# Performance work log

Measured on AMD Instinct MI355X. Metric: run time of the kernel, lower is better.

The kernel has to match this reference:

```python
import jax, jax.numpy as jnp
import numpy as np

N_SAMPLES = 32768
WINDOW = 2048
HOP = WINDOW // 2
N_FRAMES = N_SAMPLES // HOP  # 32 resonance frames
BASE_RES = 0.5
RES_SPAN = 1.0 - BASE_RES
RES_FACTOR = 0.9
N_RES = 32
EXPR = 4
CPD = 16
N_COEFFS = WINDOW // 2 + 1  # 1025


def interpolate_last_axis(x, new_size):
    # linear interpolation along last axis (align_corners=False semantics)
    old = x.shape[-1]
    pos = (jnp.arange(new_size, dtype=jnp.float32) + 0.5) * (old / new_size) - 0.5
    pos = jnp.clip(pos, 0.0, old - 1.0)
    lo = jnp.floor(pos).astype(jnp.int32)
    hi = jnp.minimum(lo + 1, old - 1)
    w = pos - lo.astype(jnp.float32)
    return x[..., lo] * (1.0 - w) + x[..., hi] * w


def overlap_add(frames):
    # frames: (..., n_frames, window); hop = window//2; output (..., n_frames*hop)
    *lead, nf, w = frames.shape
    hop = w // 2
    a = frames[..., :hop]
    b = frames[..., hop:]
    b = jnp.concatenate([jnp.zeros_like(b[..., :1, :]), b[..., :-1, :]], axis=-2)
    return (a + b).reshape(*lead, nf * hop)


def freq_domain_transfer_function_to_resonance(window_size, decay_coeffs, n_frames, start_phase, start_mags):
    # decay_coeffs/start_phase/start_mags: (nr, expr, n_coeffs); log-space decay scan
    log_decay = jnp.log(decay_coeffs + 1e-12)[..., None, :]  # (nr, expr, 1, nc)
    shape = log_decay.shape[:-2] + (n_frames, log_decay.shape[-1])
    cum = jnp.cumsum(jnp.broadcast_to(log_decay, shape), axis=-2)  # decay^(f+1)
    mags = jnp.exp(cum) * start_mags[..., None, :]
    spec = mags * jnp.exp(1j * start_phase[..., None, :])
    frames = jnp.fft.irfft(spec, n=window_size, axis=-1)  # (nr, expr, n_frames, window)
    t = jnp.arange(window_size, dtype=jnp.float32)
    hann = 0.5 - 0.5 * jnp.cos(2.0 * jnp.pi * t / window_size)
    return overlap_add(frames * hann)  # (nr, expr, n_frames*hop)


def unit_norm(x):
    return x / (jnp.linalg.norm(x, axis=-1, keepdims=True) + 1e-8)


def fft_convolve(a, b):
    n = a.shape[-1]
    fa = jnp.fft.rfft(a, n=2 * n, axis=-1)
    fb = jnp.fft.rfft(b, n=2 * n, axis=-1)
    return jnp.fft.irfft(fa * fb, n=2 * n, axis=-1)[..., :n]


def setup_inputs() -> dict:
    key = jax.random.key(0)
    ks = jax.random.split(key, 10)
    control_signal = jax.random.normal(ks[0], (2, 4, CPD, 128), dtype=jnp.float32)
    deformations = jax.random.normal(ks[1], (2, 4, EXPR, 128), dtype=jnp.float32) * 0.1
    router = jax.random.uniform(ks[2], (CPD, N_RES), minval=-1.0, maxval=1.0)

    def init_resonance(k):
        k1, k2 = jax.random.split(k)
        res = jax.random.uniform(k1, (N_RES, N_COEFFS, 1), minval=0.01, maxval=1.0)
        deform = jax.random.uniform(k2, (1, N_COEFFS, EXPR), minval=-0.02, maxval=0.02)
        return res + deform

    amp = init_resonance(ks[3])
    phase = init_resonance(ks[4])
    decay = init_resonance(ks[5])
    gains = jax.random.uniform(ks[6], (N_RES, 1), minval=0.01, maxval=1.1)
    return {"control_signal": control_signal, "deformations": deformations,
            "router": router, "amp": amp, "phase": phase, "decay": decay, "gains": gains}


def reference(control_signal, deformations, router, amp, phase, decay, gains):
    b, e, cpd, frames = control_signal.shape
    nr = router.shape[1]
    # route control plane -> resonances: (b,e,nr,frames)
    routed = jnp.einsum('becf,cr->berf', control_signal, router)
    before_upsample = routed
    # (nr, n_coeffs, expr) -> (nr, expr, n_coeffs)
    amp_t = jnp.transpose(amp, (0, 2, 1))
    phase_t = jnp.transpose(phase, (0, 2, 1))
    decay_t = jnp.transpose(decay, (0, 2, 1))
    d_coeffs = BASE_RES + jax.nn.sigmoid(decay_t) * RES_SPAN * RES_FACTOR
    res = freq_domain_transfer_function_to_resonance(
        WINDOW, d_coeffs, N_FRAMES, jnp.tanh(phase_t) * jnp.pi, jnp.abs(amp_t))
    res = unit_norm(res)[None, None]  # (1,1,nr,expr,N)
    routed_up = interpolate_last_axis(routed[:, :, :, None, :], N_SAMPLES)  # (b,e,nr,1,N)
    noise = jax.random.uniform(jax.random.key(123), routed_up.shape, minval=-1.0, maxval=1.0)
    routed_up = routed_up * noise
    conv = fft_convolve(routed_up, res)  # (b,e,nr,expr,N)
    d = deformations.at[:, :, 0, :].add(1.0)  # base deformation favors first expressivity
    d = jax.nn.softmax(d, axis=2)[:, :, None, :, :]  # (b,e,1,expr,def_frames)
    d = interpolate_last_axis(d, N_SAMPLES)
    x = jnp.sum(d * conv, axis=-2)  # mix over expressivity -> (b,e,nr,N)
    summed = jnp.tanh(x * jnp.abs(gains).reshape(1, 1, nr, 1))
    summed = jnp.sum(summed, axis=-2, keepdims=True)  # (b,e,1,N)
    return summed, before_upsample
```

## Files before the change

### kernel.cpp

```cpp
#include <hip/hip_runtime.h>
#include <hip/hip_fp16.h>
#include <stdint.h>


#define PI_F     3.14159265358979323846f
#define TWOPI_F  6.28318530717958647692f
#define UNIT64K  (TWOPI_F/65536.0f)
#define UNIT2K   (TWOPI_F/2048.0f)
#define SCALE64K (1.0f/65536.0f)
#define SK3(i)   ((i) + 3*((i) >> 4))
#define RPH 308
#define SKP(i)   ((i) + 4*((i) >> 4))
#define RPW 328

__device__ __forceinline__ float2 cmul(float2 a, float2 b){
  return make_float2(a.x*b.x - a.y*b.y, a.x*b.y + a.y*b.x);
}

__device__ __forceinline__ float2 twid(uint32_t e, float unit, float sign){
  float ang = (float)e * unit;
  float sn, cn;
  __sincosf(ang, &sn, &cn);
  return make_float2(cn, sign*sn);
}

__device__ __forceinline__ float2 mulnegi(float2 w){ return make_float2(w.y, -w.x); }
__device__ __forceinline__ float2 mulposi(float2 w){ return make_float2(-w.y, w.x); }

__device__ __forceinline__ void bfly_fwd(float2& u, float2& v, float2 w){
  float2 d = make_float2(u.x - v.x, u.y - v.y);
  u = make_float2(u.x + v.x, u.y + v.y);
  v = cmul(d, w);
}

__device__ __forceinline__ uint32_t rotl32(uint32_t v, int r){
  return (v << r) | (v >> (32 - r));
}

__device__ __forceinline__ void threefry2x32(uint32_t c0, uint32_t c1,
                                             uint32_t& o0, uint32_t& o1){
  const uint32_t k0 = 0u, k1 = 123u;
  const uint32_t k2 = 0x1BD11BDAu ^ k0 ^ k1;
  const uint32_t ks[3] = {k0, k1, k2};
  uint32_t x0 = c0 + k0, x1 = c1 + k1;
#pragma unroll
  for (int i = 0; i < 5; i++){
    if ((i & 1) == 0){
      x0 += x1; x1 = rotl32(x1,13); x1 ^= x0;
      x0 += x1; x1 = rotl32(x1,15); x1 ^= x0;
      x0 += x1; x1 = rotl32(x1,26); x1 ^= x0;
      x0 += x1; x1 = rotl32(x1, 6); x1 ^= x0;
    } else {
      x0 += x1; x1 = rotl32(x1,17); x1 ^= x0;
      x0 += x1; x1 = rotl32(x1,29); x1 ^= x0;
      x0 += x1; x1 = rotl32(x1,16); x1 ^= x0;
      x0 += x1; x1 = rotl32(x1,24); x1 ^= x0;
    }
    x0 += ks[(i+1)%3];
    x1 += ks[(i+2)%3] + (uint32_t)(i+1);
  }
  o0 = x0; o1 = x1;
}

__device__ __forceinline__ float jax_noise(uint32_t p){
  uint32_t b0, b1;
  threefry2x32(0u, p, b0, b1);
  uint32_t bits = b0 ^ b1;
  float u = __uint_as_float((bits >> 9) | 0x3f800000u) - 1.0f;
  return fmaxf(-1.0f, u*2.0f - 1.0f);
}

__device__ __forceinline__ void interp128(int t, int& lo, int& hi, float& w){
  float posf = ((float)t + 0.5f) * (1.0f/256.0f) - 0.5f;
  posf = fminf(fmaxf(posf, 0.0f), 127.0f);
  lo = (int)posf;
  hi = lo + 1; if (hi > 127) hi = 127;
  w = posf - (float)lo;
}

__device__ __forceinline__ __half2 u2h(uint32_t u){
  union { uint32_t u; __half2 h; } x; x.u = u; return x.h;
}
__device__ __forceinline__ uint32_t h2u(__half2 h){
  union { uint32_t u; __half2 h; } x; x.h = h; return x.u;
}
__device__ __forceinline__ constexpr int sw4(int k){ return ((k & 3) << 2) | (k >> 2); }
__device__ __forceinline__ constexpr int br4(int x){
  return ((x & 1) << 3) | ((x & 2) << 1) | ((x & 4) >> 1) | ((x & 8) >> 3);
}

__device__ __forceinline__ void cws(float2& u, const float c, const float s){
  const float x = u.x*c - u.y*s;
  u.y = u.x*s + u.y*c;
  u.x = x;
}
__device__ __forceinline__ void cwv(float2& u, const float2 w){
  const float x = u.x*w.x - u.y*w.y;
  u.y = u.x*w.y + u.y*w.x;
  u.x = x;
}

__device__ __forceinline__ void dft4(float2& a, float2& b, float2& c, float2& d,
                                     const float sgn){
  float2 t0 = make_float2(a.x + c.x, a.y + c.y);
  float2 t1 = make_float2(a.x - c.x, a.y - c.y);
  float2 t2 = make_float2(b.x + d.x, b.y + d.y);
  float2 t3 = make_float2(b.x - d.x, b.y - d.y);
  float2 i3 = make_float2(-sgn*t3.y, sgn*t3.x);
  a = make_float2(t0.x + t2.x, t0.y + t2.y);
  c = make_float2(t0.x - t2.x, t0.y - t2.y);
  b = make_float2(t1.x + i3.x, t1.y + i3.y);
  d = make_float2(t1.x - i3.x, t1.y - i3.y);
}

#define DFT16_TW(d, sgn) do { \
  const float C1_ = 0.92387953251128674f, S1_ = 0.38268343236508978f; \
  const float C2_ = 0.70710678118654752f; \
  cws(d[5],  C1_,  (sgn)*S1_); \
  cws(d[6],  C2_,  (sgn)*C2_); \
  cws(d[7],  S1_,  (sgn)*C1_); \
  cws(d[9],  C2_,  (sgn)*C2_); \
  cws(d[10], 0.0f, (sgn)); \
  cws(d[11], -C2_, (sgn)*C2_); \
  cws(d[13], S1_,  (sgn)*C1_); \
  cws(d[14], -C2_, (sgn)*C2_); \
  cws(d[15], -C1_, -(sgn)*S1_); \
} while(0)

__device__ __forceinline__ void dft16(float2* d, const float sgn){
#pragma unroll
  for (int nb = 0; nb < 4; nb++) dft4(d[nb], d[nb+4], d[nb+8], d[nb+12], sgn);
  DFT16_TW(d, sgn);
#pragma unroll
  for (int ka = 0; ka < 4; ka++) dft4(d[4*ka], d[4*ka+1], d[4*ka+2], d[4*ka+3], sgn);
}
__device__ __forceinline__ void dft16b(float2* d, const float sgn){
#pragma unroll
  for (int nb = 0; nb < 4; nb++) dft4(d[4*nb], d[4*nb+1], d[4*nb+2], d[4*nb+3], sgn);
  DFT16_TW(d, sgn);
#pragma unroll
  for (int ka = 0; ka < 4; ka++) dft4(d[ka], d[ka+4], d[ka+8], d[ka+12], sgn);
}

__device__ __forceinline__ void pass1_fwd(__half2* buf, const float2* twl, const int t){
  const int row = t >> 4, L = t & 15;
  __half2* BR = buf + row*RPW;
  float2 d[16];
#pragma unroll
  for (int H = 0; H < 16; H++) d[H] = __half22float2(BR[L + 20*H]);
  dft16(d, -1.0f);
#pragma unroll
  for (int k1 = 0; k1 < 16; k1++){
    float2 y = d[sw4(k1)];
    cwv(y, twl[(L*k1) & 255]);
    BR[L + 20*k1] = __floats2half2_rn(y.x, y.y);
  }
}

__global__ void k_routed(const float* __restrict__ ctrl, const float* __restrict__ defm,
                         const float* __restrict__ router,
                         float* __restrict__ w_routed, float* __restrict__ w_sm,
                         float* __restrict__ out1){
  int idx = blockIdx.x*blockDim.x + threadIdx.x;
  if (idx < 32768){
    int f = idx & 127, r = (idx >> 7) & 31, be = idx >> 12;
    float acc = 0.0f;
#pragma unroll
    for (int c = 0; c < 16; c++)
      acc += ctrl[(be*16 + c)*128 + f] * router[c*32 + r];
    w_routed[idx] = acc;
    out1[idx] = acc;
  } else if (idx < 32768 + 1024){
    int j = idx - 32768;
    int f = j & 127, be = j >> 7;
    float v[4];
#pragma unroll
    for (int x = 0; x < 4; x++)
      v[x] = defm[(be*4 + x)*128 + f] + (x == 0 ? 1.0f : 0.0f);
    float mx = fmaxf(fmaxf(v[0], v[1]), fmaxf(v[2], v[3]));
    float s = 0.0f;
#pragma unroll
    for (int x = 0; x < 4; x++){ v[x] = expf(v[x] - mx); s += v[x]; }
#pragma unroll
    for (int x = 0; x < 4; x++) w_sm[(be*4 + x)*128 + f] = v[x]/s;
  }
}

__global__ void k_frames(const float* __restrict__ amp, const float* __restrict__ phase,
                         const float* __restrict__ decay, float2* __restrict__ w_fr){
  const int wg = blockIdx.x;
  const int f = wg & 31;
  const int rp = wg >> 5;
  const int p = rp & 1;
  const int r = rp >> 1;
  const int t = threadIdx.x;
  __shared__ float2 buf[2048];

  for (int k = t; k <= 1024; k += 256){
    float2 S[2];
#pragma unroll
    for (int d = 0; d < 2; d++){
      const int x = 2*p + d;
      const int base = (r*1025 + k)*4 + x;
      float a  = fabsf(amp[base]);
      float ph = tanhf(phase[base]) * PI_F;
      float sg = 1.0f / (1.0f + expf(-decay[base]));
      float dc = 0.5f + 0.45f * sg;
      float mag = expf(logf(dc + 1e-12f) * (float)(f+1)) * a;
      float snv, csv;
      sincosf(ph, &snv, &csv);
      float re = mag * csv, im = mag * snv;
      if (k == 0 || k == 1024) im = 0.0f;
      S[d] = make_float2(re, im);
    }
    buf[__brev((uint32_t)k) >> 21] =
        make_float2(S[0].x - S[1].y, S[0].y + S[1].x);
    if (k >= 1 && k <= 1023)
      buf[__brev((uint32_t)(2048 - k)) >> 21] =
          make_float2(S[0].x + S[1].y, -S[0].y + S[1].x);
  }
  __syncthreads();
  for (int s = 10; s >= 0; s--){
    const int ls = 10 - s;
    const int hl = 1 << ls;
    for (int bi = t; bi < 1024; bi += 256){
      const int g = bi >> ls, j = bi & (hl - 1);
      const int i0 = g*2*hl + j, i1 = i0 + hl;
      float2 pp = buf[i0], qq = buf[i1];
      float2 w = twid((uint32_t)(j << s), UNIT2K, +1.0f);
      float2 v = cmul(qq, w);
      buf[i0] = make_float2(pp.x+v.x, pp.y+v.y);
      buf[i1] = make_float2(pp.x-v.x, pp.y-v.y);
    }
    __syncthreads();
  }
  float2* O = w_fr + (size_t)wg*2048;
  for (int u = t; u < 2048; u += 256){
    float hann = 0.5f - 0.5f*cosf(TWOPI_F * (float)u / 2048.0f);
    float sc = (1.0f/2048.0f) * hann;
    O[u] = make_float2(buf[u].x*sc, buf[u].y*sc);
  }
}

__global__ void k_ola(const float2* __restrict__ w_fr, float* __restrict__ w_resT,
                      float* __restrict__ w_sumsq){
  const int wg = blockIdx.x;
  const int cq = wg & 7;
  const int rp = wg >> 3;
  const int c0 = cq*32;
  const int r = rp >> 1, p = rp & 1;
  const int ch0 = r*4 + p*2;
  const int t = threadIdx.x;
  __shared__ float tx[32][129], ty[32][129];
  __shared__ float red[2][256];
  const float2* F = w_fr + (size_t)rp*32*2048;
  float acc0 = 0.0f, acc1 = 0.0f;
#pragma unroll
  for (int it = 0; it < 16; it++){
    const int idx = it*256 + t;
    const int cp = idx & 31, m = idx >> 5;
    const int n = c0 + cp + 256*m;
    const int f = n >> 10, u = n & 1023;
    float2 a = F[(size_t)f*2048 + u];
    float vx = a.x, vy = a.y;
    if (f > 0){
      float2 b = F[(size_t)(f-1)*2048 + u + 1024];
      vx += b.x; vy += b.y;
    }
    tx[cp][m] = vx; ty[cp][m] = vy;
    acc0 += vx*vx; acc1 += vy*vy;
  }
  red[0][t] = acc0; red[1][t] = acc1;
  __syncthreads();
#pragma unroll
  for (int it = 0; it < 16; it++){
    const int idx = it*256 + t;
    const int m = idx & 127, cp = idx >> 7;
    w_resT[(size_t)ch0*32768 + (size_t)(c0+cp)*128 + m]     = tx[cp][m];
    w_resT[(size_t)(ch0+1)*32768 + (size_t)(c0+cp)*128 + m] = ty[cp][m];
  }
  for (int off = 128; off > 0; off >>= 1){
    __syncthreads();
    if (t < off){ red[0][t] += red[0][t+off]; red[1][t] += red[1][t+off]; }
  }
  if (t == 0){
    atomicAdd(&w_sumsq[ch0],     red[0][0]);
    atomicAdd(&w_sumsq[ch0 + 1], red[1][0]);
  }
}

__global__ void k_norm(const float* __restrict__ w_sumsq, float* __restrict__ w_invnorm){
  const int s = threadIdx.x;
  if (s < 128) w_invnorm[s] = 1.0f/(sqrtf(w_sumsq[s]) + 1e-8f);
}

__global__ void k_fwdA(const int mode, const float* __restrict__ w_resT,
                       const float* __restrict__ w_invnorm,
                       const float* __restrict__ w_routed,
                       __half2* __restrict__ outh){
  const int wg = blockIdx.x;
  const int cq = wg & 63;
  const int sig = wg >> 6;
  const int c0 = cq*4;
  const int t = threadIdx.x;
  __shared__ __half2 buf[4][RPH];
  if (mode == 0){
    const int rr = sig >> 1, pq = sig & 1;
    const int ch0 = rr*4 + pq*2;
    const float inv0 = w_invnorm[ch0], inv1 = w_invnorm[ch0+1];
#pragma unroll
    for (int i = 0; i < 2; i++){
      const int j = i*256 + t;
      const int cc = j & 3, m = j >> 2;
      const int c = c0 + cc;
      float vx = w_resT[(size_t)ch0*32768 + c*128 + m] * inv0;
      float vy = w_resT[(size_t)(ch0+1)*32768 + c*128 + m] * inv1;
      buf[cc][SK3(m)] = __floats2half2_rn(vx, vy);
      buf[cc][SK3(m + 128)] = __floats2half2_rn(0.0f, 0.0f);
    }
  } else {
    const float* rp = w_routed + sig*128;
#pragma unroll
    for (int i = 0; i < 2; i++){
      const int j = i*256 + t;
      const int cc = j & 3, m = j >> 2;
      const int c = c0 + cc;
      const int n = c + 256*m;
      int lo, hi; float w;
      interp128(n, lo, hi, w);
      float rv = rp[lo]*(1.0f - w) + rp[hi]*w;
      float vx = rv * jax_noise((uint32_t)sig*32768u + (uint32_t)n);
      buf[cc][SK3(m)] = __floats2half2_rn(vx, 0.0f);
      buf[cc][SK3(m + 128)] = __floats2half2_rn(0.0f, 0.0f);
    }
  }
  __syncthreads();
  const int row = t >> 6, q = t & 63;
  for (int sp = 0; sp < 4; sp++){
    const int s  = 2*sp;
    const int hh = 1 << (6 - 2*sp);
    const int hl = hh << 1;
    const int lj = 6 - 2*sp;
    const int j = q & (hh - 1), g = q >> lj;
    const int base = g*2*hl + j;
    const uint32_t e = (uint32_t)(c0 + row) + 256u*(uint32_t)j;
    __half2* B = buf[row];
    const int i0 = SK3(base), i1 = SK3(base+hh), i2 = SK3(base+hl), i3 = SK3(base+hl+hh);
    float2 u0 = __half22float2(B[i0]);
    float2 u1 = __half22float2(B[i1]);
    float2 u2 = __half22float2(B[i2]);
    float2 u3 = __half22float2(B[i3]);
    float2 wA0 = twid((e << s) & 0xFFFFu, UNIT64K, -1.0f);
    float2 wA1 = mulnegi(wA0);
    float2 wB  = cmul(wA0, wA0);
    bfly_fwd(u0, u2, wA0);
    bfly_fwd(u1, u3, wA1);
    bfly_fwd(u0, u1, wB);
    bfly_fwd(u2, u3, wB);
    B[i0] = __floats2half2_rn(u0.x, u0.y);
    B[i1] = __floats2half2_rn(u1.x, u1.y);
    B[i2] = __floats2half2_rn(u2.x, u2.y);
    B[i3] = __floats2half2_rn(u3.x, u3.y);
    __syncthreads();
  }
#pragma unroll
  for (int i = 0; i < 4; i++){
    const int cc = i, m = t;
    outh[(size_t)sig*65536 + (size_t)(c0+cc)*256 + m] = buf[cc][SK3(m)];
  }
}

__global__ __launch_bounds__(256, 4)
void k_fwdB(const __half2* __restrict__ spech, __half2* __restrict__ resp_t){
  const int wg = blockIdx.x;
  const int mq = wg & 15;
  const int sig = wg >> 4;
  const int m16 = mq*16;
  const int t = threadIdx.x;
  __shared__ alignas(16) __half2 buf[16*RPW];
  __shared__ float2 twl[256];
  twl[t] = twid((uint32_t)t << 8, UNIT64K, -1.0f);
  const __half2* base = spech + (size_t)sig*65536;
  {
    const int mm = t & 15, q = t >> 4;
    __half2* BR = buf + mm*RPW;
#pragma unroll
    for (int i = 0; i < 16; i++)
      BR[20*i + q] = base[(size_t)(16*i + q)*256 + m16 + mm];
  }
  __syncthreads();
  pass1_fwd(buf, twl, t);
  __syncthreads();
  {
    const int k1 = t >> 4, row = t & 15;
    __half2* BG = buf + row*RPW + 20*k1;
    float2 v[16];
#pragma unroll
    for (int cc = 0; cc < 4; cc++){
      const uint4 ld = *reinterpret_cast<const uint4*>(BG + 4*cc);
      v[4*cc+0] = __half22float2(u2h(ld.x));
      v[4*cc+1] = __half22float2(u2h(ld.y));
      v[4*cc+2] = __half22float2(u2h(ld.z));
      v[4*cc+3] = __half22float2(u2h(ld.w));
    }
    dft16(v, -1.0f);
    uint4* O4 = reinterpret_cast<uint4*>(resp_t + (((size_t)sig*16 + mq)*256 + t)*16);
#pragma unroll
    for (int cc = 0; cc < 4; cc++){
      uint4 st;
      st.x = h2u(__floats2half2_rn(v[4*cc+0].x, v[4*cc+0].y));
      st.y = h2u(__floats2half2_rn(v[4*cc+1].x, v[4*cc+1].y));
      st.z = h2u(__floats2half2_rn(v[4*cc+2].x, v[4*cc+2].y));
      st.w = h2u(__floats2half2_rn(v[4*cc+3].x, v[4*cc+3].y));
      O4[cc] = st;
    }
  }
}

__global__ __launch_bounds__(256, 4)
void k_conv(const __half2* __restrict__ ruspec,
            const __half2* __restrict__ resp_t,
            __half2* __restrict__ chunkbuf, const int gbase){
  const int wg = blockIdx.x;
  const int mq = wg & 15;
  const int p  = (wg >> 4) & 1;
  const int gl = wg >> 5;
  const int g = gbase + gl;
  const int r = g & 31;
  const int m16 = mq*16;
  const int t = threadIdx.x;
  __shared__ alignas(16) __half2 buf[16*RPW];
  __shared__ float2 twl[256];
  twl[t] = twid((uint32_t)t << 8, UNIT64K, -1.0f);

  {
    const uint4* A4 = reinterpret_cast<const uint4*>(
        ruspec + (size_t)g*65536 + (size_t)t*256 + m16);
    uint4 a0 = A4[0], a1 = A4[1], a2 = A4[2], a3 = A4[3];
    const int cs = SKP(t);
    uint32_t w[16];
    w[0]=a0.x; w[1]=a0.y; w[2]=a0.z; w[3]=a0.w;
    w[4]=a1.x; w[5]=a1.y; w[6]=a1.z; w[7]=a1.w;
    w[8]=a2.x; w[9]=a2.y; w[10]=a2.z; w[11]=a2.w;
    w[12]=a3.x; w[13]=a3.y; w[14]=a3.z; w[15]=a3.w;
#pragma unroll
    for (int mm = 0; mm < 16; mm++)
      buf[mm*RPW + cs] = u2h(w[mm]);
  }
  __syncthreads();
  pass1_fwd(buf, twl, t);
  __syncthreads();
  {
    const int k1 = t >> 4, row = t & 15;
    __half2* BG = buf + row*RPW + 20*k1;
    float2 v[16];
#pragma unroll
    for (int cc = 0; cc < 4; cc++){
      const uint4 ld = *reinterpret_cast<const uint4*>(BG + 4*cc);
      v[4*cc+0] = __half22float2(u2h(ld.x));
      v[4*cc+1] = __half22float2(u2h(ld.y));
      v[4*cc+2] = __half22float2(u2h(ld.z));
      v[4*cc+3] = __half22float2(u2h(ld.w));
    }
    const uint4* Bt = reinterpret_cast<const uint4*>(
        resp_t + (((size_t)(r*2 + p)*16 + mq)*256 + t)*16);
    uint4 b0 = Bt[0], b1 = Bt[1], b2 = Bt[2], b3 = Bt[3];
    dft16(v, -1.0f);
    uint32_t bw[16];
    bw[0]=b0.x; bw[1]=b0.y; bw[2]=b0.z; bw[3]=b0.w;
    bw[4]=b1.x; bw[5]=b1.y; bw[6]=b1.z; bw[7]=b1.w;
    bw[8]=b2.x; bw[9]=b2.y; bw[10]=b2.z; bw[11]=b2.w;
    bw[12]=b3.x; bw[13]=b3.y; bw[14]=b3.z; bw[15]=b3.w;
#pragma unroll
    for (int pp = 0; pp < 16; pp++){
      const float2 b = __half22float2(u2h(bw[pp]));
      const float zx = v[pp].x, zy = v[pp].y;
      v[pp] = make_float2((zx*b.x - zy*b.y)*SCALE64K,
                          (zx*b.y + zy*b.x)*SCALE64K);
    }
    dft16b(v, +1.0f);
    __half2 h[16];
#pragma unroll
    for (int n2 = 0; n2 < 16; n2++){
      float2 m = v[n2];
      const float2 w = twl[(n2*k1) & 255];
      const float x = m.x*w.x + m.y*w.y;
      m.y = -m.x*w.y + m.y*w.x;
      m.x = x;
      h[n2] = __floats2half2_rn(m.x, m.y);
    }
#pragma unroll
    for (int cc = 0; cc < 4; cc++){
      uint4 st;
      st.x = h2u(h[4*cc+0]);
      st.y = h2u(h[4*cc+1]);
      st.z = h2u(h[4*cc+2]);
      st.w = h2u(h[4*cc+3]);
      *reinterpret_cast<uint4*>(BG + 4*cc) = st;
    }
  }
  __syncthreads();
  {
    const int row = t >> 4, L = t & 15;
    __half2* BR = buf + row*RPW;
    float2 d[16];
#pragma unroll
    for (int k1 = 0; k1 < 16; k1++) d[k1] = __half22float2(BR[L + 20*k1]);
    dft16(d, +1.0f);
#pragma unroll
    for (int H = 0; H < 16; H++){
      const float2 x = d[sw4(H)];
      BR[L + 20*H] = __floats2half2_rn(x.x, x.y);
    }
  }
  __syncthreads();
  {
    uint4* O4 = reinterpret_cast<uint4*>(
        chunkbuf + (size_t)(gl*2 + p)*65536 + (size_t)t*256 + m16);
    const int cs = SKP(t);
#pragma unroll
    for (int q4 = 0; q4 < 4; q4++){
      uint4 st;
      st.x = h2u(buf[(4*q4+0)*RPW + cs]);
      st.y = h2u(buf[(4*q4+1)*RPW + cs]);
      st.z = h2u(buf[(4*q4+2)*RPW + cs]);
      st.w = h2u(buf[(4*q4+3)*RPW + cs]);
      O4[q4] = st;
    }
  }
}

__global__ __launch_bounds__(256, 4)
void k_invA_w(const __half2* __restrict__ chunkbuf, const int gbase,
              const float* __restrict__ w_sm, const float* __restrict__ gains,
              float* __restrict__ out0){
  const int wg = blockIdx.x;
  const int c8 = wg & 31;
  const int gl = wg >> 5;
  const int g = gbase + gl;
  const int r = g & 31, be = g >> 5;
  const int c0 = c8*8;
  const int t = threadIdx.x;
  __shared__ alignas(16) __half2 buf[16*RPW];
  __shared__ float sm_lds[512];
  sm_lds[t]       = w_sm[be*512 + t];
  sm_lds[256 + t] = w_sm[be*512 + 256 + t];

  const int row = t >> 4;
  const int p   = row >> 3;
  const int cc  = row & 7;
  const int c   = c0 + cc;
  {
    const int u = t & 15;
    const uint4* C4 = reinterpret_cast<const uint4*>(
        chunkbuf + (size_t)(gl*2 + p)*65536 + (size_t)c*256 + 16*br4(u));
    uint4 z0 = C4[0], z1 = C4[1], z2 = C4[2], z3 = C4[3];
    uint32_t zw[16];
    zw[0]=z0.x; zw[1]=z0.y; zw[2]=z0.z; zw[3]=z0.w;
    zw[4]=z1.x; zw[5]=z1.y; zw[6]=z1.z; zw[7]=z1.w;
    zw[8]=z2.x; zw[9]=z2.y; zw[10]=z2.z; zw[11]=z2.w;
    zw[12]=z3.x; zw[13]=z3.y; zw[14]=z3.z; zw[15]=z3.w;
    const float2 wstep = twid((uint32_t)(16*c) & 0xFFFFu, UNIT64K, +1.0f);
    float2 w = make_float2(1.0f, 0.0f);
    float2 d[16];
#pragma unroll
    for (int rh = 0; rh < 16; rh++){
      d[rh] = cmul(__half22float2(u2h(zw[br4(rh)])), w);
      w = cmul(w, wstep);
    }
    dft16(d, +1.0f);
    __half2* BR = buf + row*RPW;
#pragma unroll
    for (int mL = 0; mL < 16; mL++){
      const float2 s = d[sw4(mL)];
      BR[20*mL + u] = __floats2half2_rn(s.x, s.y);
    }
  }
  __syncthreads();
  const int mL = t & 15;
  float2 v[16];
  {
    const __half2* BG = buf + row*RPW + 20*mL;
#pragma unroll
    for (int q4 = 0; q4 < 4; q4++){
      const uint4 ld = *reinterpret_cast<const uint4*>(BG + 4*q4);
      v[4*q4+0] = __half22float2(u2h(ld.x));
      v[4*q4+1] = __half22float2(u2h(ld.y));
      v[4*q4+2] = __half22float2(u2h(ld.z));
      v[4*q4+3] = __half22float2(u2h(ld.w));
    }
  }
  __syncthreads();
  {
    const float2 wstep = twid((uint32_t)(c + 256*mL) & 0xFFFFu, UNIT64K, +1.0f);
    float2 w = wstep;
#pragma unroll
    for (int kL2 = 1; kL2 < 16; kL2++){
      v[kL2] = cmul(v[kL2], w);
      w = cmul(w, wstep);
    }
    dft16(v, +1.0f);
    __half2* BR = buf + row*RPW;
#pragma unroll
    for (int mH = 0; mH < 8; mH++){
      const float2 x = v[sw4(mH)];
      BR[mL + 20*mH] = __floats2half2_rn(x.x, x.y);
    }
  }
  __syncthreads();
  const float gv = fabsf(gains[r]);
#pragma unroll
  for (int it = 0; it < 4; it++){
    const int li = t + it*256;
    const int cc2 = li & 7, m = li >> 3;
    const int tt = c0 + cc2 + 256*m;
    int lo, hi; float w;
    interp128(tt, lo, hi, w);
    const int cell = (m & 15) + 20*(m >> 4);
    float2 z0 = __half22float2(buf[cc2*RPW + cell]);
    float2 z1 = __half22float2(buf[(8 + cc2)*RPW + cell]);
    float dw0 = sm_lds[0*128 + lo]*(1.0f - w) + sm_lds[0*128 + hi]*w;
    float dw1 = sm_lds[1*128 + lo]*(1.0f - w) + sm_lds[1*128 + hi]*w;
    float dw2 = sm_lds[2*128 + lo]*(1.0f - w) + sm_lds[2*128 + hi]*w;
    float dw3 = sm_lds[3*128 + lo]*(1.0f - w) + sm_lds[3*128 + hi]*w;
    float val = dw0*z0.x + dw1*z0.y + dw2*z1.x + dw3*z1.y;
    atomicAdd(&out0[(size_t)be*32768 + tt], tanhf(val*gv));
  }
}

extern "C" void kernel_launch(void* const* d_in, const int* in_sizes, int n_in,
                              void* d_out, int out_size, void* d_ws, size_t ws_size,
                              hipStream_t stream){
  const float* ctrl   = (const float*)d_in[0];
  const float* defm   = (const float*)d_in[1];
  const float* router = (const float*)d_in[2];
  const float* amp    = (const float*)d_in[3];
  const float* phase  = (const float*)d_in[4];
  const float* decay  = (const float*)d_in[5];
  const float* gains  = (const float*)d_in[6];
  float* out = (float*)d_out;
  float* ws  = (float*)d_ws;

  float*   w_resT    = ws;
  float*   w_routed  = ws + 4194304;
  float*   w_sm      = ws + 4227072;
  float*   w_invnorm = ws + 4231168;
  float*   w_sumsq   = ws + 4231296;
  __half2* ruspec_h  = (__half2*)(ws + 4231424);
  __half2* resp_h    = (__half2*)(ws + 21008640);
  __half2* chunk_h   = (__half2*)(ws + 25202944);
  const size_t base_f = 25202944;
  float2* w_fr       = (float2*)ruspec_h;
  __half2* resp_t    = (__half2*)w_resT;

  int G = 0;
  for (int gg = 128; gg >= 1; gg >>= 1){
    size_t need = (base_f + (size_t)gg*131072) * sizeof(float);
    if (need <= ws_size){ G = gg; break; }
  }

  hipMemsetAsync(d_out, 0, 262144*sizeof(float), stream);
  k_routed<<<132, 256, 0, stream>>>(ctrl, defm, router, w_routed, w_sm, out + 262144);
  if (G == 0) return;

  hipMemsetAsync(w_sumsq, 0, 128*sizeof(float), stream);
  k_frames<<<2048, 256, 0, stream>>>(amp, phase, decay, w_fr);
  k_ola<<<512, 256, 0, stream>>>(w_fr, w_resT, w_sumsq);
  k_norm<<<1, 128, 0, stream>>>(w_sumsq, w_invnorm);
  k_fwdA<<<64*64, 256, 0, stream>>>(0, w_resT, w_invnorm, w_routed, resp_h);
  k_fwdB<<<64*16, 256, 0, stream>>>(resp_h, resp_t);
  k_fwdA<<<256*64, 256, 0, stream>>>(1, w_resT, w_invnorm, w_routed, ruspec_h);
  for (int gb = 0; gb < 256; gb += G){
    k_conv<<<G*32, 256, 0, stream>>>(ruspec_h, resp_t, chunk_h, gb);
    k_invA_w<<<G*32, 256, 0, stream>>>(chunk_h, gb, w_sm, gains, out);
  }
}
```

Measured before the change: 343.8 us.

## Rewrite k_fwdA as register radix-16 two-pass FFT over 16 columns per block

Replaces the shared-memory radix-4 butterfly loop (four passes with a barrier each, one sincos per butterfly) in k_fwdA with a register-resident radix-16 DFT pair. Each thread does a 16-point DFT with incremental twiddles, one shared-memory transpose, a second 16-point DFT, and vectorised uint4 stores. Each block now covers 16 columns instead of 4, so the grid shrinks fourfold. This cuts barriers, LDS traffic and transcendental calls, at the cost of higher register pressure (launch bounds 256,4) and twiddles that accumulate by repeated multiplication, which slightly changes rounding.

```diff
diff --git a/kernel.cpp b/kernel.cpp
--- a/kernel.cpp
+++ b/kernel.cpp
@@ -8,8 +8,6 @@
 #define UNIT64K  (TWOPI_F/65536.0f)
 #define UNIT2K   (TWOPI_F/2048.0f)
 #define SCALE64K (1.0f/65536.0f)
-#define SK3(i)   ((i) + 3*((i) >> 4))
-#define RPH 308
 #define SKP(i)   ((i) + 4*((i) >> 4))
 #define RPW 328
 
@@ -22,15 +20,6 @@
   float sn, cn;
   __sincosf(ang, &sn, &cn);
   return make_float2(cn, sign*sn);
-}
-
-__device__ __forceinline__ float2 mulnegi(float2 w){ return make_float2(w.y, -w.x); }
-__device__ __forceinline__ float2 mulposi(float2 w){ return make_float2(-w.y, w.x); }
-
-__device__ __forceinline__ void bfly_fwd(float2& u, float2& v, float2 w){
-  float2 d = make_float2(u.x - v.x, u.y - v.y);
-  u = make_float2(u.x + v.x, u.y + v.y);
-  v = cmul(d, w);
 }
 
 __device__ __forceinline__ uint32_t rotl32(uint32_t v, int r){
@@ -294,79 +283,98 @@
   if (s < 128) w_invnorm[s] = 1.0f/(sqrtf(w_sumsq[s]) + 1e-8f);
 }
 
-__global__ void k_fwdA(const int mode, const float* __restrict__ w_resT,
-                       const float* __restrict__ w_invnorm,
-                       const float* __restrict__ w_routed,
-                       __half2* __restrict__ outh){
+__global__ __launch_bounds__(256, 4)
+void k_fwdA(const int mode, const float* __restrict__ w_resT,
+            const float* __restrict__ w_invnorm,
+            const float* __restrict__ w_routed,
+            __half2* __restrict__ outh){
   const int wg = blockIdx.x;
-  const int cq = wg & 63;
-  const int sig = wg >> 6;
-  const int c0 = cq*4;
+  const int cq = wg & 15;
+  const int sig = wg >> 4;
   const int t = threadIdx.x;
-  __shared__ __half2 buf[4][RPH];
-  if (mode == 0){
-    const int rr = sig >> 1, pq = sig & 1;
-    const int ch0 = rr*4 + pq*2;
-    const float inv0 = w_invnorm[ch0], inv1 = w_invnorm[ch0+1];
-#pragma unroll
-    for (int i = 0; i < 2; i++){
-      const int j = i*256 + t;
-      const int cc = j & 3, m = j >> 2;
-      const int c = c0 + cc;
-      float vx = w_resT[(size_t)ch0*32768 + c*128 + m] * inv0;
-      float vy = w_resT[(size_t)(ch0+1)*32768 + c*128 + m] * inv1;
-      buf[cc][SK3(m)] = __floats2half2_rn(vx, vy);
-      buf[cc][SK3(m + 128)] = __floats2half2_rn(0.0f, 0.0f);
-    }
-  } else {
-    const float* rp = w_routed + sig*128;
-#pragma unroll
-    for (int i = 0; i < 2; i++){
-      const int j = i*256 + t;
-      const int cc = j & 3, m = j >> 2;
-      const int c = c0 + cc;
-      const int n = c + 256*m;
-      int lo, hi; float w;
-      interp128(n, lo, hi, w);
-      float rv = rp[lo]*(1.0f - w) + rp[hi]*w;
-      float vx = rv * jax_noise((uint32_t)sig*32768u + (uint32_t)n);
-      buf[cc][SK3(m)] = __floats2half2_rn(vx, 0.0f);
-      buf[cc][SK3(m + 128)] = __floats2half2_rn(0.0f, 0.0f);
-    }
-  }
-  __syncthreads();
-  const int row = t >> 6, q = t & 63;
-  for (int sp = 0; sp < 4; sp++){
-    const int s  = 2*sp;
-    const int hh = 1 << (6 - 2*sp);
-    const int hl = hh << 1;
-    const int lj = 6 - 2*sp;
-    const int j = q & (hh - 1), g = q >> lj;
-    const int base = g*2*hl + j;
-    const uint32_t e = (uint32_t)(c0 + row) + 256u*(uint32_t)j;
-    __half2* B = buf[row];
-    const int i0 = SK3(base), i1 = SK3(base+hh), i2 = SK3(base+hl), i3 = SK3(base+hl+hh);
-    float2 u0 = __half22float2(B[i0]);
-    float2 u1 = __half22float2(B[i1]);
-    float2 u2 = __half22float2(B[i2]);
-    float2 u3 = __half22float2(B[i3]);
-    float2 wA0 = twid((e << s) & 0xFFFFu, UNIT64K, -1.0f);
-    float2 wA1 = mulnegi(wA0);
-    float2 wB  = cmul(wA0, wA0);
-    bfly_fwd(u0, u2, wA0);
-    bfly_fwd(u1, u3, wA1);
-    bfly_fwd(u0, u1, wB);
-    bfly_fwd(u2, u3, wB);
-    B[i0] = __floats2half2_rn(u0.x, u0.y);
-    B[i1] = __floats2half2_rn(u1.x, u1.y);
-    B[i2] = __floats2half2_rn(u2.x, u2.y);
-    B[i3] = __floats2half2_rn(u3.x, u3.y);
-    __syncthreads();
-  }
-#pragma unroll
-  for (int i = 0; i < 4; i++){
-    const int cc = i, m = t;
-    outh[(size_t)sig*65536 + (size_t)(c0+cc)*256 + m] = buf[cc][SK3(m)];
+  const int cc = t >> 4;
+  const int c  = cq*16 + cc;
+  __shared__ alignas(16) __half2 buf[16*RPW];
+
+  {
+    const int mL = t & 15;
+    float2 d[16];
+    if (mode == 0){
+      const int rr = sig >> 1, pq = sig & 1;
+      const int ch0 = rr*4 + pq*2;
+      const float inv0 = w_invnorm[ch0], inv1 = w_invnorm[ch0+1];
+      const float* X0 = w_resT + (size_t)ch0*32768 + (size_t)c*128;
+      const float* X1 = w_resT + (size_t)(ch0+1)*32768 + (size_t)c*128;
+#pragma unroll
+      for (int mH = 0; mH < 8; mH++){
+        const int m = mL + 16*mH;
+        d[mH] = make_float2(X0[m]*inv0, X1[m]*inv1);
+      }
+#pragma unroll
+      for (int mH = 8; mH < 16; mH++) d[mH] = make_float2(0.0f, 0.0f);
+    } else {
+      const float* rp = w_routed + sig*128;
+#pragma unroll
+      for (int mH = 0; mH < 8; mH++){
+        const int m = mL + 16*mH;
+        const int n = c + 256*m;
+        int lo, hi; float w;
+        interp128(n, lo, hi, w);
+        float rv = rp[lo]*(1.0f - w) + rp[hi]*w;
+        d[mH] = make_float2(rv * jax_noise((uint32_t)sig*32768u + (uint32_t)n), 0.0f);
+      }
+#pragma unroll
+      for (int mH = 8; mH < 16; mH++) d[mH] = make_float2(0.0f, 0.0f);
+    }
+    dft16(d, -1.0f);
+    const float2 wstep = twid((uint32_t)(c + 256*mL) & 0xFFFFu, UNIT64K, -1.0f);
+    float2 w = wstep;
+    __half2* BR = buf + cc*RPW;
+    BR[mL] = __floats2half2_rn(d[0].x, d[0].y);
+#pragma unroll
+    for (int rl = 1; rl < 16; rl++){
+      float2 y = d[sw4(rl)];
+      cwv(y, w);
+      w = cmul(w, wstep);
+      BR[20*rl + mL] = __floats2half2_rn(y.x, y.y);
+    }
+  }
+  __syncthreads();
+  {
+    const int rl = t & 15;
+    const __half2* BG = buf + cc*RPW + 20*rl;
+    float2 v[16];
+#pragma unroll
+    for (int q4 = 0; q4 < 4; q4++){
+      const uint4 ld = *reinterpret_cast<const uint4*>(BG + 4*q4);
+      v[4*q4+0] = __half22float2(u2h(ld.x));
+      v[4*q4+1] = __half22float2(u2h(ld.y));
+      v[4*q4+2] = __half22float2(u2h(ld.z));
+      v[4*q4+3] = __half22float2(u2h(ld.w));
+    }
+    dft16(v, -1.0f);
+    const float2 wstep = twid((uint32_t)(16*c) & 0xFFFFu, UNIT64K, -1.0f);
+    float2 w = wstep;
+    __half2 y[16];
+    y[0] = __floats2half2_rn(v[0].x, v[0].y);
+#pragma unroll
+    for (int rh = 1; rh < 16; rh++){
+      float2 u = v[sw4(rh)];
+      cwv(u, w);
+      w = cmul(w, wstep);
+      y[rh] = __floats2half2_rn(u.x, u.y);
+    }
+    uint4* O4 = reinterpret_cast<uint4*>(
+        outh + (size_t)sig*65536 + (size_t)c*256 + 16*br4(rl));
+#pragma unroll
+    for (int q4 = 0; q4 < 4; q4++){
+      uint4 st;
+      st.x = h2u(y[br4(4*q4+0)]);
+      st.y = h2u(y[br4(4*q4+1)]);
+      st.z = h2u(y[br4(4*q4+2)]);
+      st.w = h2u(y[br4(4*q4+3)]);
+      O4[q4] = st;
+    }
   }
 }
 
@@ -667,9 +675,9 @@
   k_frames<<<2048, 256, 0, stream>>>(amp, phase, decay, w_fr);
   k_ola<<<512, 256, 0, stream>>>(w_fr, w_resT, w_sumsq);
   k_norm<<<1, 128, 0, stream>>>(w_sumsq, w_invnorm);
-  k_fwdA<<<64*64, 256, 0, stream>>>(0, w_resT, w_invnorm, w_routed, resp_h);
+  k_fwdA<<<64*16, 256, 0, stream>>>(0, w_resT, w_invnorm, w_routed, resp_h);
   k_fwdB<<<64*16, 256, 0, stream>>>(resp_h, resp_t);
-  k_fwdA<<<256*64, 256, 0, stream>>>(1, w_resT, w_invnorm, w_routed, ruspec_h);
+  k_fwdA<<<256*16, 256, 0, stream>>>(1, w_resT, w_invnorm, w_routed, ruspec_h);
   for (int gb = 0; gb < 256; gb += G){
     k_conv<<<G*32, 256, 0, stream>>>(ruspec_h, resp_t, chunk_h, gb);
     k_invA_w<<<G*32, 256, 0, stream>>>(chunk_h, gb, w_sm, gains, out);
```

Measured after the change: 345.0 us. Within noise of the previous version (+0.3%).
